# Kernel tuning notes

Measured on AMD Instinct MI355X. Metric: run time of the kernel, lower is better.

The kernel has to match this reference:

```python
import jax, jax.numpy as jnp
import numpy as np

# Model constants (match init_kwargs)
H, P, N, G, NL, K = 32, 64, 128, 1, 15, 4   # heads, head_dim, state, groups, lambda levels, conv width
HID, T, BATCH = 1024, 1024, 1
INTER = H * P                    # 2048
CONV_DIM = INTER + 2 * G * N     # 2304
PROJ = INTER + CONV_DIM + H * (NL + 1)  # 4864
EPS = 1e-5


def _level_matrix(t_len: int) -> np.ndarray:
    """Fenwick-tree level assignment: for query t, prefix [0,t] splits into
    power-of-two segments from binary expansion of t+1; segment of length 2^l -> level l."""
    lm = np.zeros((t_len, t_len), dtype=np.int32)
    for t in range(t_len):
        n = t + 1
        while n > 0:
            lb = n & (-n)
            lm[t, n - lb:n] = lb.bit_length() - 1
            n -= lb
    return lm


def setup_inputs() -> dict:
    key = jax.random.key(0)
    ks = jax.random.split(key, 4)
    return {
        "hidden_states": jax.random.normal(ks[0], (BATCH, T, HID), jnp.float32),
        "in_proj_w": jax.random.normal(ks[1], (PROJ, HID), jnp.float32) / np.sqrt(HID).astype(np.float32),
        "in_proj_b": jnp.zeros((PROJ,), jnp.float32),
        "conv_w": jax.random.normal(ks[2], (CONV_DIM, K), jnp.float32) / np.sqrt(K).astype(np.float32),
        "dt_bias": jnp.ones((H,), jnp.float32),
        "A_log": jnp.log(jnp.arange(1, H + 1, dtype=jnp.float32)),
        "L_param": jnp.ones((H, NL), jnp.float32),
        "D": jnp.ones((H,), jnp.float32),
        "rmsnorm_w": jnp.ones((INTER,), jnp.float32),
        "out_proj_w": jax.random.normal(ks[3], (HID, INTER), jnp.float32) / np.sqrt(INTER).astype(np.float32),
        "out_proj_b": jnp.zeros((HID,), jnp.float32),
        "level_mat": jnp.asarray(_level_matrix(T)),  # (T,T) int32, data-independent
    }


def reference(hidden_states, in_proj_w, in_proj_b, conv_w, dt_bias, A_log,
              L_param, D, rmsnorm_w, out_proj_w, out_proj_b, level_mat):
    b, t, _ = hidden_states.shape
    # in_proj and split: [z | xBC | dt | dl]
    zxbcdtdl = hidden_states @ in_proj_w.T + in_proj_b
    z, xBC, dt, dl = jnp.split(zxbcdtdl, [INTER, INTER + CONV_DIM, INTER + CONV_DIM + H], axis=-1)
    # depthwise causal conv1d (width K) + SiLU
    xp = jnp.pad(xBC, ((0, 0), (K - 1, 0), (0, 0)))
    conv = sum(xp[:, w:w + t, :] * conv_w[:, w] for w in range(K))
    xBC = jax.nn.silu(conv)
    x, Bm, Cm = jnp.split(xBC, [INTER, INTER + G * N], axis=-1)
    x = x.reshape(b, t, H, P)          # v pre-scale
    Bm = Bm.reshape(b, t, G, N)        # keys
    Cm = Cm.reshape(b, t, G, N)        # queries
    dl = dl.reshape(b, t, H, NL)
    # D residual uses unscaled x (matches hmamba_chunk_scan_combined ordering)
    D_res = x * D[None, None, :, None]
    dt = jax.nn.softplus(dt + dt_bias)            # (b,t,H)
    v = x * dt[..., None]                          # (b,t,H,P)
    A = -jnp.exp(A_log)                            # (H,)
    g = A * dt                                     # (b,t,H), per-token log-decay (<=0)
    Ls = jax.nn.softplus(L_param * dl)             # (b,t,H,NL) per-token level scales
    # cumulative log-decay; decay(t,s) = exp(cg_t - cg_s), s<=t
    cg = jnp.cumsum(g, axis=1).transpose(0, 2, 1)  # (b,H,t)
    mask = jnp.tril(jnp.ones((t, t), bool))
    logdecay = jnp.where(mask, cg[:, :, :, None] - cg[:, :, None, :], -jnp.inf)
    decay = jnp.exp(logdecay)                      # (b,H,t,s)
    # hierarchical level scale H[t,s] = Ls[b,t,h, level(t,s)]
    Hmat = jnp.take_along_axis(Ls.transpose(0, 2, 1, 3), level_mat[None, None, :, :], axis=-1)  # (b,H,t,s)
    scores = jnp.einsum('btgn,bsgn->bgts', Cm, Bm)  # (b,G,t,s), G=1 broadcasts over heads
    att = scores * decay * Hmat                     # (b,H,t,s), masked via decay=0
    y = jnp.einsum('bhts,bshp->bthp', att, v) + D_res
    y = y.reshape(b, t, INTER)
    # gated RMSNorm with norm_before_gate=False: normalize(y * silu(z)) * w
    yg = y * jax.nn.silu(z)
    y = yg * jax.lax.rsqrt(jnp.mean(yg * yg, axis=-1, keepdims=True) + EPS) * rmsnorm_w
    return y @ out_proj_w.T + out_proj_b
```

## Files before the change

### kernel.cpp

```cpp
#include <hip/hip_runtime.h>
#include <hip/hip_bf16.h>
#include <math.h>

#define T_LEN 1024
#define HID 1024
#define NHEAD 32
#define HDIM 64
#define NSTATE 128
#define NLVL 15
#define KCONV 4
#define INTER 2048
#define CONV_DIM 2304
#define PROJ 4864
#define NPROJ16 4352
#define NPROJF 512
#define EPS 1e-5f

typedef __attribute__((ext_vector_type(8))) _Float16 half8;
typedef __attribute__((ext_vector_type(4))) float float4v;
typedef unsigned short ushort_t;

__device__ __forceinline__ float softplus_f(float x) {
  return fmaxf(x, 0.f) + log1pf(expf(-fabsf(x)));
}
__device__ __forceinline__ float silu_f(float x) {
  return x / (1.f + expf(-x));
}
__device__ __forceinline__ ushort_t f2h(float f) {
  union { _Float16 h; ushort_t u; } v;
  v.h = (_Float16)f;
  return v.u;
}
__device__ __forceinline__ float h2f(ushort_t u) {
  union { ushort_t u; _Float16 h; } v;
  v.u = u;
  return (float)v.h;
}
__device__ __forceinline__ void gload_lds16(const void* g, void* l) {
  __builtin_amdgcn_global_load_lds(
      (const __attribute__((address_space(1))) void*)g,
      (__attribute__((address_space(3))) void*)l, 16, 0, 0);
}

#define N4_HS  (T_LEN * HID / 4)
#define N4_WI  (PROJ * HID / 4)
#define N4_WO  (HID * INTER / 4)
__global__ __launch_bounds__(256) void prep_f16(
    const float* __restrict__ hs, const float* __restrict__ wi,
    const float* __restrict__ wo, ushort_t* __restrict__ hsb,
    ushort_t* __restrict__ wib, ushort_t* __restrict__ wob) {
  int i = blockIdx.x * 256 + threadIdx.x;
  const float* src; ushort_t* dst; int j;
  if (i < N4_HS)              { src = hs; dst = hsb; j = i; }
  else if (i < N4_HS + N4_WI) { src = wi; dst = wib; j = i - N4_HS; }
  else                        { src = wo; dst = wob; j = i - N4_HS - N4_WI; }
  float4 v = reinterpret_cast<const float4*>(src)[j];
  union { ushort_t u[4]; unsigned long long ll; } o;
  o.u[0] = f2h(v.x); o.u[1] = f2h(v.y); o.u[2] = f2h(v.z); o.u[3] = f2h(v.w);
  reinterpret_cast<unsigned long long*>(dst)[j] = o.ll;
}

__global__ __launch_bounds__(256) void gemm_in(
    const ushort_t* __restrict__ A, const ushort_t* __restrict__ B,
    const float* __restrict__ bias,
    ushort_t* __restrict__ Ch, float* __restrict__ Cf) {
  const int K = HID;
  __shared__ ushort_t As[2][128][32];
  __shared__ ushort_t Bs[2][128][32];
  const int tid = threadIdx.x;
  const int w = tid >> 6, L = tid & 63;
  const int n0 = blockIdx.x * 128, m0 = blockIdx.y * 128;
  const int mq = (w & 1) * 64, nq = (w >> 1) * 64;
  const int srow = (L >> 2);
  const int sch = (L & 3) * 8;

  float4v acc[4][4];
#pragma unroll
  for (int i = 0; i < 4; ++i)
#pragma unroll
    for (int j = 0; j < 4; ++j) acc[i][j] = (float4v){0.f, 0.f, 0.f, 0.f};

  const int niter = K / 32;
  {
#pragma unroll
    for (int j = 0; j < 2; ++j) {
      int r0 = 16 * (w * 2 + j);
      gload_lds16(A + (size_t)(m0 + r0 + srow) * K + sch, &As[0][r0][0]);
      gload_lds16(B + (size_t)(n0 + r0 + srow) * K + sch, &Bs[0][r0][0]);
    }
  }
  for (int it = 0; it < niter; ++it) {
    __syncthreads();
    if (it + 1 < niter) {
      const int kk = (it + 1) * 32;
      const int nb = (it + 1) & 1;
#pragma unroll
      for (int j = 0; j < 2; ++j) {
        int r0 = 16 * (w * 2 + j);
        gload_lds16(A + (size_t)(m0 + r0 + srow) * K + kk + sch, &As[nb][r0][0]);
        gload_lds16(B + (size_t)(n0 + r0 + srow) * K + kk + sch, &Bs[nb][r0][0]);
      }
    }
    const int cb = it & 1;
    half8 af[4], bf[4];
#pragma unroll
    for (int t = 0; t < 4; ++t) {
      af[t] = *reinterpret_cast<const half8*>(&As[cb][mq + t * 16 + (L & 15)][(L >> 4) * 8]);
      bf[t] = *reinterpret_cast<const half8*>(&Bs[cb][nq + t * 16 + (L & 15)][(L >> 4) * 8]);
    }
#pragma unroll
    for (int mt = 0; mt < 4; ++mt)
#pragma unroll
      for (int nt = 0; nt < 4; ++nt)
        acc[mt][nt] = __builtin_amdgcn_mfma_f32_16x16x32_f16(af[mt], bf[nt], acc[mt][nt], 0, 0, 0);
  }
  const int qrow = (L >> 4) * 4;
  const bool tof16 = (n0 < NPROJ16);
#pragma unroll
  for (int mt = 0; mt < 4; ++mt) {
#pragma unroll
    for (int nt = 0; nt < 4; ++nt) {
      int col = n0 + nq + nt * 16 + (L & 15);
      float bv = bias[col];
#pragma unroll
      for (int r = 0; r < 4; ++r) {
        int row = m0 + mq + mt * 16 + qrow + r;
        float v = acc[mt][nt][r] + bv;
        if (tof16) Ch[(size_t)row * NPROJ16 + col] = f2h(v);
        else       Cf[(size_t)row * NPROJF + (col - NPROJ16)] = v;
      }
    }
  }
}

__global__ __launch_bounds__(256) void gemm_f16_sk(
    const ushort_t* __restrict__ A, const ushort_t* __restrict__ B,
    float* __restrict__ Cpart, int M, int N, int K, int Kc) {
  __shared__ ushort_t As[2][128][32];
  __shared__ ushort_t Bs[2][128][32];
  const int tid = threadIdx.x;
  const int w = tid >> 6, L = tid & 63;
  const int n0 = blockIdx.x * 128, m0 = blockIdx.y * 128;
  const int kbeg = blockIdx.z * Kc;
  float* __restrict__ C = Cpart + (size_t)blockIdx.z * M * N;
  const int mq = (w & 1) * 64, nq = (w >> 1) * 64;
  const int srow = (L >> 2);
  const int sch = (L & 3) * 8;

  float4v acc[4][4];
#pragma unroll
  for (int i = 0; i < 4; ++i)
#pragma unroll
    for (int j = 0; j < 4; ++j) acc[i][j] = (float4v){0.f, 0.f, 0.f, 0.f};

  const int niter = Kc / 32;
  {
    const int kk = kbeg;
#pragma unroll
    for (int j = 0; j < 2; ++j) {
      int r0 = 16 * (w * 2 + j);
      gload_lds16(A + (size_t)(m0 + r0 + srow) * K + kk + sch, &As[0][r0][0]);
      gload_lds16(B + (size_t)(n0 + r0 + srow) * K + kk + sch, &Bs[0][r0][0]);
    }
  }
  for (int it = 0; it < niter; ++it) {
    __syncthreads();
    if (it + 1 < niter) {
      const int kk = kbeg + (it + 1) * 32;
      const int nb = (it + 1) & 1;
#pragma unroll
      for (int j = 0; j < 2; ++j) {
        int r0 = 16 * (w * 2 + j);
        gload_lds16(A + (size_t)(m0 + r0 + srow) * K + kk + sch, &As[nb][r0][0]);
        gload_lds16(B + (size_t)(n0 + r0 + srow) * K + kk + sch, &Bs[nb][r0][0]);
      }
    }
    const int cb = it & 1;
    half8 af[4], bf[4];
#pragma unroll
    for (int t = 0; t < 4; ++t) {
      af[t] = *reinterpret_cast<const half8*>(&As[cb][mq + t * 16 + (L & 15)][(L >> 4) * 8]);
      bf[t] = *reinterpret_cast<const half8*>(&Bs[cb][nq + t * 16 + (L & 15)][(L >> 4) * 8]);
    }
#pragma unroll
    for (int mt = 0; mt < 4; ++mt)
#pragma unroll
      for (int nt = 0; nt < 4; ++nt)
        acc[mt][nt] = __builtin_amdgcn_mfma_f32_16x16x32_f16(af[mt], bf[nt], acc[mt][nt], 0, 0, 0);
  }
  const int qrow = (L >> 4) * 4;
#pragma unroll
  for (int mt = 0; mt < 4; ++mt) {
#pragma unroll
    for (int nt = 0; nt < 4; ++nt) {
      int col = n0 + nq + nt * 16 + (L & 15);
#pragma unroll
      for (int r = 0; r < 4; ++r) {
        int row = m0 + mq + mt * 16 + qrow + r;
        C[(size_t)row * N + col] = acc[mt][nt][r];
      }
    }
  }
}

__global__ __launch_bounds__(256) void reduce_out4(const float* __restrict__ p,
                                                   const float* __restrict__ bias,
                                                   float* __restrict__ out, int MN) {
  int i = blockIdx.x * 256 + threadIdx.x;
  if (i * 4 >= MN) return;
  float4 a = reinterpret_cast<const float4*>(p)[i];
  float4 b = reinterpret_cast<const float4*>(p + MN)[i];
  float4 c = reinterpret_cast<const float4*>(p + 2 * (size_t)MN)[i];
  float4 d = reinterpret_cast<const float4*>(p + 3 * (size_t)MN)[i];
  int col = (i * 4) & (HID - 1);
  float4 bv = *reinterpret_cast<const float4*>(bias + col);
  float4 o;
  o.x = a.x + b.x + c.x + d.x + bv.x;
  o.y = a.y + b.y + c.y + d.y + bv.y;
  o.z = a.z + b.z + c.z + d.z + bv.z;
  o.w = a.w + b.w + c.w + d.w + bv.w;
  reinterpret_cast<float4*>(out)[i] = o;
}

__global__ __launch_bounds__(512) void pointwise_dt(
    const float* __restrict__ zxf, const float* __restrict__ dt_bias,
    const float* __restrict__ A_log, const float* __restrict__ L_param,
    float* __restrict__ dtbuf, float* __restrict__ gT,
    float* __restrict__ Lsbuf) {
  const int t = blockIdx.x;
  const int j = threadIdx.x;
  const size_t ro = (size_t)t * NPROJF;
  if (j < NHEAD * NLVL) {
    float x = L_param[j] * zxf[ro + NHEAD + j];
    Lsbuf[(size_t)t * (NHEAD * NLVL) + j] = softplus_f(x);
  } else {
    int h = j - NHEAD * NLVL;
    float x = zxf[ro + h] + dt_bias[h];
    float dt = softplus_f(x);
    dtbuf[t * NHEAD + h] = dt;
    gT[h * T_LEN + t] = -expf(A_log[h]) * dt;
  }
}

__global__ __launch_bounds__(64) void scan_g(const float* __restrict__ gT,
                                             double* __restrict__ cgd) {
  const int h = blockIdx.x, l = threadIdx.x;
  const float* gr = gT + (size_t)h * T_LEN + l * 16;
  double pre[16];
  double acc = 0.0;
#pragma unroll
  for (int i = 0; i < 16; ++i) { acc += (double)gr[i]; pre[i] = acc; }
  double s = acc;
#pragma unroll
  for (int off = 1; off < 64; off <<= 1) {
    double o = __shfl_up(s, off, 64);
    if (l >= off) s += o;
  }
  const double base = s - acc;
  double* cr = cgd + (size_t)h * T_LEN + l * 16;
#pragma unroll
  for (int i = 0; i < 16; ++i) cr[i] = base + pre[i];
}

__global__ __launch_bounds__(256) void conv_fused(
    const ushort_t* __restrict__ zxh, const float* __restrict__ conv_w,
    const float* __restrict__ dtbuf, const float* __restrict__ Dp,
    ushort_t* __restrict__ vt, float* __restrict__ ybuf,
    ushort_t* __restrict__ Bb, ushort_t* __restrict__ Cb) {
  __shared__ ushort_t Vl[64][68];
  __shared__ float dtl[64];
  const int tq = blockIdx.x, cy = blockIdx.y;
  const int t0 = tq * 64;
  const int tid = threadIdx.x;
  const int lane = tid & 63, g = tid >> 6;
  const bool vpath = (cy < 32);
  const int ccol = vpath ? cy * 64 + lane : INTER + (cy - 32) * 64 + lane;
  const int zcol = INTER + ccol;
  float cw[KCONV];
#pragma unroll
  for (int w = 0; w < KCONV; ++w) cw[w] = conv_w[ccol * KCONV + w];
  if (vpath && tid < 64) dtl[tid] = dtbuf[(t0 + tid) * NHEAD + cy];
  const float Dh = vpath ? Dp[cy] : 0.f;

  float xv[19];
#pragma unroll
  for (int i = 0; i < 19; ++i) {
    int tt = t0 + g * 16 - 3 + i;
    if (tt >= 0) {
      xv[i] = h2f(zxh[(size_t)tt * NPROJ16 + zcol]);
    } else xv[i] = 0.f;
  }
  __syncthreads();
#pragma unroll
  for (int i = 0; i < 16; ++i) {
    float acc = xv[i] * cw[0] + xv[i + 1] * cw[1] + xv[i + 2] * cw[2] + xv[i + 3] * cw[3];
    float sil = silu_f(acc);
    int tl = g * 16 + i;
    int t = t0 + tl;
    if (vpath) {
      ushort_t vh = f2h(sil * dtl[tl]);
      Vl[tl][lane] = vh;
      ybuf[(size_t)t * INTER + cy * 64 + lane] = sil * Dh;
    } else if (ccol < INTER + NSTATE) {
      Bb[t * NSTATE + (ccol - INTER)] = f2h(sil);
    } else {
      Cb[t * NSTATE + (ccol - INTER - NSTATE)] = f2h(sil);
    }
  }
  if (vpath) {
    __syncthreads();
#pragma unroll
    for (int rep = 0; rep < 2; ++rep) {
      int u = tid + 256 * rep;
      int p = u >> 3, t8 = (u & 7) * 8;
      union { ushort_t u16[8]; half8 h; } o;
#pragma unroll
      for (int j = 0; j < 8; ++j) o.u16[j] = Vl[t8 + j][p];
      *reinterpret_cast<half8*>(vt + (size_t)(cy * 64 + p) * T_LEN + t0 + t8) = o.h;
    }
  }
}

__global__ __launch_bounds__(256) void attn_mfma(
    const ushort_t* __restrict__ Bb, const ushort_t* __restrict__ Cb,
    const ushort_t* __restrict__ vt, const double* __restrict__ cgd,
    const float* __restrict__ Lsb, float* __restrict__ ybuf) {
  __shared__ ushort_t Bl[64][136];
  __shared__ ushort_t Vtl[64][72];
  __shared__ ushort_t Sl[64][72];
  __shared__ float Lsl[64][16];
  __shared__ float cgq[64];
  __shared__ float cgs[64];

  const int item = blockIdx.x;
  const int h = item / 40;
  const int rem = item - h * 40;
  int qt, j;
  if (rem < 4)        { qt = rem;                 j = 0; }
  else if (rem < 12)  { qt = 4 + (rem - 4) / 2;   j = (rem - 4) % 2; }
  else if (rem < 24)  { qt = 8 + (rem - 12) / 3;  j = (rem - 12) % 3; }
  else                { qt = 12 + (rem - 24) / 4; j = (rem - 24) % 4; }

  const int tid = threadIdx.x;
  const int w = tid >> 6, L = tid & 63;
  const int tq0 = qt * 64;
  const double* cgh = cgd + (size_t)h * T_LEN;
  const double base = cgh[tq0];

  for (int i = tid; i < 64 * NLVL; i += 256) {
    int r = i / NLVL, l = i - r * NLVL;
    Lsl[r][l] = Lsb[(size_t)(tq0 + r) * (NHEAD * NLVL) + h * NLVL + l];
  }
  if (tid < 64) cgq[tid] = (float)(cgh[tq0 + tid] - base);

  half8 cfrag[4];
  {
    const ushort_t* cr = Cb + (size_t)(tq0 + w * 16 + (L & 15)) * NSTATE + (L >> 4) * 8;
#pragma unroll
    for (int ks = 0; ks < 4; ++ks)
      cfrag[ks] = *reinterpret_cast<const half8*>(cr + ks * 32);
  }
  float4v yac[4];
#pragma unroll
  for (int i = 0; i < 4; ++i) yac[i] = (float4v){0.f, 0.f, 0.f, 0.f};

  const int qrow = w * 16 + ((L >> 4) << 2);

  const int st0 = 4 * j;
  const int st1 = min(4 * j + 4, qt + 1);
  for (int st = st0; st < st1; ++st) {
    const int ts0 = st * 64;
    __syncthreads();
#pragma unroll
    for (int i = 0; i < 4; ++i) {
      int u = tid + 256 * i;
      int row = u >> 4, kb = (u & 15) * 8;
      *reinterpret_cast<half8*>(&Bl[row][kb]) =
          *reinterpret_cast<const half8*>(Bb + (size_t)(ts0 + row) * NSTATE + kb);
    }
#pragma unroll
    for (int i = 0; i < 2; ++i) {
      int u = tid + 256 * i;
      int p = u >> 3, sc = (u & 7) * 8;
      *reinterpret_cast<half8*>(&Vtl[p][sc]) =
          *reinterpret_cast<const half8*>(vt + (size_t)(h * HDIM + p) * T_LEN + ts0 + sc);
    }
    if (tid < 64) cgs[tid] = (float)(cgh[ts0 + tid] - base);
    __syncthreads();

    float4v sac[4];
#pragma unroll
    for (int nt = 0; nt < 4; ++nt) sac[nt] = (float4v){0.f, 0.f, 0.f, 0.f};
#pragma unroll
    for (int ks = 0; ks < 4; ++ks) {
#pragma unroll
      for (int nt = 0; nt < 4; ++nt) {
        half8 bfrag = *reinterpret_cast<const half8*>(&Bl[nt * 16 + (L & 15)][ks * 32 + (L >> 4) * 8]);
        sac[nt] = __builtin_amdgcn_mfma_f32_16x16x32_f16(cfrag[ks], bfrag, sac[nt], 0, 0, 0);
      }
    }
#pragma unroll
    for (int nt = 0; nt < 4; ++nt) {
      int s = nt * 16 + (L & 15);
      int sg = ts0 + s;
      float cs = cgs[s];
#pragma unroll
      for (int r = 0; r < 4; ++r) {
        int q = qrow + r;
        int tg = tq0 + q;
        float val = 0.f;
        if (sg <= tg) {
          int lvl = 31 - __clz((unsigned)(sg ^ (tg + 1)));
          val = sac[nt][r] * __expf(cgq[q] - cs) * Lsl[q][lvl];
        }
        Sl[q][s] = f2h(val);
      }
    }
    __builtin_amdgcn_s_waitcnt(0);
#pragma unroll
    for (int ks = 0; ks < 2; ++ks) {
      half8 af = *reinterpret_cast<const half8*>(&Sl[w * 16 + (L & 15)][ks * 32 + (L >> 4) * 8]);
#pragma unroll
      for (int pt = 0; pt < 4; ++pt) {
        half8 bfv = *reinterpret_cast<const half8*>(&Vtl[pt * 16 + (L & 15)][ks * 32 + (L >> 4) * 8]);
        yac[pt] = __builtin_amdgcn_mfma_f32_16x16x32_f16(af, bfv, yac[pt], 0, 0, 0);
      }
    }
  }
#pragma unroll
  for (int pt = 0; pt < 4; ++pt) {
    int p = pt * 16 + (L & 15);
#pragma unroll
    for (int r = 0; r < 4; ++r) {
      int q = qrow + r;
      atomicAdd(ybuf + (size_t)(tq0 + q) * INTER + h * HDIM + p, yac[pt][r]);
    }
  }
}

__global__ __launch_bounds__(256) void rmsnorm_gate(
    const float* __restrict__ ybuf, const ushort_t* __restrict__ zxh,
    const float* __restrict__ w, ushort_t* __restrict__ yhf) {
  __shared__ float red[4];
  const int t = blockIdx.x, tid = threadIdx.x;
  const size_t ro = (size_t)t * NPROJ16;
  const float* yrow = ybuf + (size_t)t * INTER;
  float yg[8];
  float ss = 0.f;
#pragma unroll
  for (int i = 0; i < 8; ++i) {
    int c = tid + 256 * i;
    float z = h2f(zxh[ro + c]);
    float g = yrow[c] * silu_f(z);
    yg[i] = g;
    ss += g * g;
  }
#pragma unroll
  for (int off = 32; off; off >>= 1) ss += __shfl_down(ss, off, 64);
  if ((tid & 63) == 0) red[tid >> 6] = ss;
  __syncthreads();
  if (tid == 0) red[0] = red[0] + red[1] + red[2] + red[3];
  __syncthreads();
  const float scale = rsqrtf(red[0] / (float)INTER + EPS);
#pragma unroll
  for (int i = 0; i < 8; ++i) {
    int c = tid + 256 * i;
    yhf[(size_t)t * INTER + c] = f2h(yg[i] * scale * w[c]);
  }
}

extern "C" void kernel_launch(void* const* d_in, const int* in_sizes, int n_in,
                              void* d_out, int out_size, void* d_ws, size_t ws_size,
                              hipStream_t stream) {
  const float* hs        = (const float*)d_in[0];
  const float* in_proj_w = (const float*)d_in[1];
  const float* in_proj_b = (const float*)d_in[2];
  const float* conv_w    = (const float*)d_in[3];
  const float* dt_bias   = (const float*)d_in[4];
  const float* A_log     = (const float*)d_in[5];
  const float* L_param   = (const float*)d_in[6];
  const float* Dp        = (const float*)d_in[7];
  const float* rms_w     = (const float*)d_in[8];
  const float* out_proj_w= (const float*)d_in[9];
  const float* out_proj_b= (const float*)d_in[10];
  float* out = (float*)d_out;

  char* W = (char*)d_ws;
  size_t off = 0;
  auto alloc = [&](size_t bytes) { void* p = W + off; off = (off + bytes + 255) & ~(size_t)255; return p; };
  double*   cgd = (double*)  alloc((size_t)NHEAD * T_LEN * 8);
  float*    zxf = (float*)   alloc((size_t)T_LEN * NPROJF * 4);
  float*    opp = (float*)   alloc((size_t)4 * T_LEN * HID * 4);
  float*    ybuf= (float*)   alloc((size_t)T_LEN * INTER * 4);
  float*    gT  = (float*)   alloc((size_t)NHEAD * T_LEN * 4);
  float*    dtb = (float*)   alloc((size_t)T_LEN * NHEAD * 4);
  float*    Lsb = (float*)   alloc((size_t)T_LEN * NHEAD * NLVL * 4);
  ushort_t* zxh = (ushort_t*)alloc((size_t)T_LEN * NPROJ16 * 2);
  ushort_t* hsb = (ushort_t*)alloc((size_t)T_LEN * HID * 2);
  ushort_t* Wib = (ushort_t*)alloc((size_t)PROJ * HID * 2);
  ushort_t* Wob = (ushort_t*)alloc((size_t)HID * INTER * 2);
  ushort_t* yhf = (ushort_t*)alloc((size_t)T_LEN * INTER * 2);
  ushort_t* vt  = (ushort_t*)alloc((size_t)T_LEN * INTER * 2);
  ushort_t* Bb  = (ushort_t*)alloc((size_t)T_LEN * NSTATE * 2);
  ushort_t* Cb  = (ushort_t*)alloc((size_t)T_LEN * NSTATE * 2);

  prep_f16<<<(N4_HS + N4_WI + N4_WO) / 256, 256, 0, stream>>>(
      hs, in_proj_w, out_proj_w, hsb, Wib, Wob);

  gemm_in<<<dim3(PROJ / 128, T_LEN / 128), 256, 0, stream>>>(
      hsb, Wib, in_proj_b, zxh, zxf);

  pointwise_dt<<<T_LEN, 512, 0, stream>>>(zxf, dt_bias, A_log, L_param, dtb, gT, Lsb);

  scan_g<<<NHEAD, 64, 0, stream>>>(gT, cgd);

  conv_fused<<<dim3(T_LEN / 64, 36), 256, 0, stream>>>(
      zxh, conv_w, dtb, Dp, vt, ybuf, Bb, Cb);

  attn_mfma<<<NHEAD * 40, 256, 0, stream>>>(Bb, Cb, vt, cgd, Lsb, ybuf);

  rmsnorm_gate<<<T_LEN, 256, 0, stream>>>(ybuf, zxh, rms_w, yhf);

  gemm_f16_sk<<<dim3(HID / 128, T_LEN / 128, 4), 256, 0, stream>>>(
      yhf, Wob, opp, T_LEN, HID, INTER, INTER / 4);
  reduce_out4<<<(T_LEN * HID / 4 + 255) / 256, 256, 0, stream>>>(
      opp, out_proj_b, out, T_LEN * HID);
}
```

Before: 206.0 us.

## Hoist shared C·B score GEMM out of per-head attention and widen GEMM K-tiles

Because G=1, the C·B^T score matrix is identical across all 32 heads. It is now computed once by a new qk_gemm kernel into a T×T fp16 buffer, and attn_mfma reads it directly into registers instead of recomputing it per head. The masked decay/level scaling is done in registers, which removes the LDS round trip through Sl. Separately, both dense GEMMs move to 64-wide K tiles with an XOR-swizzled LDS layout to halve the number of barriers and avoid bank conflicts. The trade-offs are an extra launch, a 2MB intermediate buffer re-read by every head, and higher LDS use per GEMM block.

```diff
diff --git a/kernel.cpp b/kernel.cpp
--- a/kernel.cpp
+++ b/kernel.cpp
@@ -65,14 +65,14 @@
     const float* __restrict__ bias,
     ushort_t* __restrict__ Ch, float* __restrict__ Cf) {
   const int K = HID;
-  __shared__ ushort_t As[2][128][32];
-  __shared__ ushort_t Bs[2][128][32];
+  __shared__ ushort_t As[2][128][64];
+  __shared__ ushort_t Bs[2][128][64];
   const int tid = threadIdx.x;
   const int w = tid >> 6, L = tid & 63;
   const int n0 = blockIdx.x * 128, m0 = blockIdx.y * 128;
   const int mq = (w & 1) * 64, nq = (w >> 1) * 64;
-  const int srow = (L >> 2);
-  const int sch = (L & 3) * 8;
+  const int srow = L >> 3;
+  const int swst = ((L & 7) ^ srow) * 8;
 
   float4v acc[4][4];
 #pragma unroll
@@ -80,39 +80,46 @@
 #pragma unroll
     for (int j = 0; j < 4; ++j) acc[i][j] = (float4v){0.f, 0.f, 0.f, 0.f};
 
-  const int niter = K / 32;
+  const int niter = K / 64;
   {
 #pragma unroll
-    for (int j = 0; j < 2; ++j) {
-      int r0 = 16 * (w * 2 + j);
-      gload_lds16(A + (size_t)(m0 + r0 + srow) * K + sch, &As[0][r0][0]);
-      gload_lds16(B + (size_t)(n0 + r0 + srow) * K + sch, &Bs[0][r0][0]);
+    for (int j = 0; j < 4; ++j) {
+      int r0 = 8 * (w * 4 + j);
+      gload_lds16(A + (size_t)(m0 + r0 + srow) * K + swst, &As[0][r0][0]);
+      gload_lds16(B + (size_t)(n0 + r0 + srow) * K + swst, &Bs[0][r0][0]);
     }
   }
   for (int it = 0; it < niter; ++it) {
     __syncthreads();
     if (it + 1 < niter) {
-      const int kk = (it + 1) * 32;
+      const int kk = (it + 1) * 64;
       const int nb = (it + 1) & 1;
 #pragma unroll
-      for (int j = 0; j < 2; ++j) {
-        int r0 = 16 * (w * 2 + j);
-        gload_lds16(A + (size_t)(m0 + r0 + srow) * K + kk + sch, &As[nb][r0][0]);
-        gload_lds16(B + (size_t)(n0 + r0 + srow) * K + kk + sch, &Bs[nb][r0][0]);
+      for (int j = 0; j < 4; ++j) {
+        int r0 = 8 * (w * 4 + j);
+        gload_lds16(A + (size_t)(m0 + r0 + srow) * K + kk + swst, &As[nb][r0][0]);
+        gload_lds16(B + (size_t)(n0 + r0 + srow) * K + kk + swst, &Bs[nb][r0][0]);
       }
     }
     const int cb = it & 1;
-    half8 af[4], bf[4];
-#pragma unroll
-    for (int t = 0; t < 4; ++t) {
-      af[t] = *reinterpret_cast<const half8*>(&As[cb][mq + t * 16 + (L & 15)][(L >> 4) * 8]);
-      bf[t] = *reinterpret_cast<const half8*>(&Bs[cb][nq + t * 16 + (L & 15)][(L >> 4) * 8]);
-    }
-#pragma unroll
-    for (int mt = 0; mt < 4; ++mt)
-#pragma unroll
-      for (int nt = 0; nt < 4; ++nt)
-        acc[mt][nt] = __builtin_amdgcn_mfma_f32_16x16x32_f16(af[mt], bf[nt], acc[mt][nt], 0, 0, 0);
+    half8 af[4][2], bf[4][2];
+#pragma unroll
+    for (int kk2 = 0; kk2 < 2; ++kk2) {
+      const int sw = ((kk2 * 4 + (L >> 4)) ^ (L & 7)) * 8;
+#pragma unroll
+      for (int t = 0; t < 4; ++t) {
+        af[t][kk2] = *reinterpret_cast<const half8*>(&As[cb][mq + t * 16 + (L & 15)][sw]);
+        bf[t][kk2] = *reinterpret_cast<const half8*>(&Bs[cb][nq + t * 16 + (L & 15)][sw]);
+      }
+    }
+#pragma unroll
+    for (int kk2 = 0; kk2 < 2; ++kk2)
+#pragma unroll
+      for (int mt = 0; mt < 4; ++mt)
+#pragma unroll
+        for (int nt = 0; nt < 4; ++nt)
+          acc[mt][nt] = __builtin_amdgcn_mfma_f32_16x16x32_f16(af[mt][kk2], bf[nt][kk2],
+                                                               acc[mt][nt], 0, 0, 0);
   }
   const int qrow = (L >> 4) * 4;
   const bool tof16 = (n0 < NPROJ16);
@@ -136,16 +143,16 @@
 __global__ __launch_bounds__(256) void gemm_f16_sk(
     const ushort_t* __restrict__ A, const ushort_t* __restrict__ B,
     float* __restrict__ Cpart, int M, int N, int K, int Kc) {
-  __shared__ ushort_t As[2][128][32];
-  __shared__ ushort_t Bs[2][128][32];
+  __shared__ ushort_t As[2][128][64];
+  __shared__ ushort_t Bs[2][128][64];
   const int tid = threadIdx.x;
   const int w = tid >> 6, L = tid & 63;
   const int n0 = blockIdx.x * 128, m0 = blockIdx.y * 128;
   const int kbeg = blockIdx.z * Kc;
   float* __restrict__ C = Cpart + (size_t)blockIdx.z * M * N;
   const int mq = (w & 1) * 64, nq = (w >> 1) * 64;
-  const int srow = (L >> 2);
-  const int sch = (L & 3) * 8;
+  const int srow = L >> 3;
+  const int swst = ((L & 7) ^ srow) * 8;
 
   float4v acc[4][4];
 #pragma unroll
@@ -153,40 +160,46 @@
 #pragma unroll
     for (int j = 0; j < 4; ++j) acc[i][j] = (float4v){0.f, 0.f, 0.f, 0.f};
 
-  const int niter = Kc / 32;
+  const int niter = Kc / 64;
   {
-    const int kk = kbeg;
-#pragma unroll
-    for (int j = 0; j < 2; ++j) {
-      int r0 = 16 * (w * 2 + j);
-      gload_lds16(A + (size_t)(m0 + r0 + srow) * K + kk + sch, &As[0][r0][0]);
-      gload_lds16(B + (size_t)(n0 + r0 + srow) * K + kk + sch, &Bs[0][r0][0]);
+#pragma unroll
+    for (int j = 0; j < 4; ++j) {
+      int r0 = 8 * (w * 4 + j);
+      gload_lds16(A + (size_t)(m0 + r0 + srow) * K + kbeg + swst, &As[0][r0][0]);
+      gload_lds16(B + (size_t)(n0 + r0 + srow) * K + kbeg + swst, &Bs[0][r0][0]);
     }
   }
   for (int it = 0; it < niter; ++it) {
     __syncthreads();
     if (it + 1 < niter) {
-      const int kk = kbeg + (it + 1) * 32;
+      const int kk = kbeg + (it + 1) * 64;
       const int nb = (it + 1) & 1;
 #pragma unroll
-      for (int j = 0; j < 2; ++j) {
-        int r0 = 16 * (w * 2 + j);
-        gload_lds16(A + (size_t)(m0 + r0 + srow) * K + kk + sch, &As[nb][r0][0]);
-        gload_lds16(B + (size_t)(n0 + r0 + srow) * K + kk + sch, &Bs[nb][r0][0]);
+      for (int j = 0; j < 4; ++j) {
+        int r0 = 8 * (w * 4 + j);
+        gload_lds16(A + (size_t)(m0 + r0 + srow) * K + kk + swst, &As[nb][r0][0]);
+        gload_lds16(B + (size_t)(n0 + r0 + srow) * K + kk + swst, &Bs[nb][r0][0]);
       }
     }
     const int cb = it & 1;
-    half8 af[4], bf[4];
-#pragma unroll
-    for (int t = 0; t < 4; ++t) {
-      af[t] = *reinterpret_cast<const half8*>(&As[cb][mq + t * 16 + (L & 15)][(L >> 4) * 8]);
-      bf[t] = *reinterpret_cast<const half8*>(&Bs[cb][nq + t * 16 + (L & 15)][(L >> 4) * 8]);
-    }
-#pragma unroll
-    for (int mt = 0; mt < 4; ++mt)
-#pragma unroll
-      for (int nt = 0; nt < 4; ++nt)
-        acc[mt][nt] = __builtin_amdgcn_mfma_f32_16x16x32_f16(af[mt], bf[nt], acc[mt][nt], 0, 0, 0);
+    half8 af[4][2], bf[4][2];
+#pragma unroll
+    for (int kk2 = 0; kk2 < 2; ++kk2) {
+      const int sw = ((kk2 * 4 + (L >> 4)) ^ (L & 7)) * 8;
+#pragma unroll
+      for (int t = 0; t < 4; ++t) {
+        af[t][kk2] = *reinterpret_cast<const half8*>(&As[cb][mq + t * 16 + (L & 15)][sw]);
+        bf[t][kk2] = *reinterpret_cast<const half8*>(&Bs[cb][nq + t * 16 + (L & 15)][sw]);
+      }
+    }
+#pragma unroll
+    for (int kk2 = 0; kk2 < 2; ++kk2)
+#pragma unroll
+      for (int mt = 0; mt < 4; ++mt)
+#pragma unroll
+        for (int nt = 0; nt < 4; ++nt)
+          acc[mt][nt] = __builtin_amdgcn_mfma_f32_16x16x32_f16(af[mt][kk2], bf[nt][kk2],
+                                                               acc[mt][nt], 0, 0, 0);
   }
   const int qrow = (L >> 4) * 4;
 #pragma unroll
@@ -321,16 +334,61 @@
   }
 }
 
+__global__ __launch_bounds__(256) void qk_gemm(
+    const ushort_t* __restrict__ Cq, const ushort_t* __restrict__ Bk,
+    ushort_t* __restrict__ S) {
+  const int idx = blockIdx.x;
+  int qt = (int)(0.5f * (sqrtf(8.f * (float)idx + 1.f) - 1.f));
+  if ((qt + 1) * (qt + 2) / 2 <= idx) ++qt;
+  if (qt * (qt + 1) / 2 > idx) --qt;
+  const int st = idx - qt * (qt + 1) / 2;
+  const int tid = threadIdx.x, w = tid >> 6, L = tid & 63;
+  const int q0 = qt * 64 + (w & 1) * 32;
+  const int s0 = st * 64 + (w >> 1) * 32;
+
+  half8 af[2][4], bf[2][4];
+#pragma unroll
+  for (int mt = 0; mt < 2; ++mt)
+#pragma unroll
+    for (int ks = 0; ks < 4; ++ks) {
+      af[mt][ks] = *reinterpret_cast<const half8*>(
+          Cq + (size_t)(q0 + mt * 16 + (L & 15)) * NSTATE + ks * 32 + (L >> 4) * 8);
+      bf[mt][ks] = *reinterpret_cast<const half8*>(
+          Bk + (size_t)(s0 + mt * 16 + (L & 15)) * NSTATE + ks * 32 + (L >> 4) * 8);
+    }
+  float4v acc[2][2];
+#pragma unroll
+  for (int i = 0; i < 2; ++i)
+#pragma unroll
+    for (int j = 0; j < 2; ++j) acc[i][j] = (float4v){0.f, 0.f, 0.f, 0.f};
+#pragma unroll
+  for (int ks = 0; ks < 4; ++ks)
+#pragma unroll
+    for (int mt = 0; mt < 2; ++mt)
+#pragma unroll
+      for (int nt = 0; nt < 2; ++nt)
+        acc[mt][nt] = __builtin_amdgcn_mfma_f32_16x16x32_f16(af[mt][ks], bf[nt][ks],
+                                                             acc[mt][nt], 0, 0, 0);
+  const int qrow = (L >> 4) * 4;
+#pragma unroll
+  for (int mt = 0; mt < 2; ++mt)
+#pragma unroll
+    for (int nt = 0; nt < 2; ++nt) {
+      int col = s0 + nt * 16 + (L & 15);
+#pragma unroll
+      for (int r = 0; r < 4; ++r)
+        S[(size_t)(q0 + mt * 16 + qrow + r) * T_LEN + col] = f2h(acc[mt][nt][r]);
+    }
+}
+
 __global__ __launch_bounds__(256) void attn_mfma(
-    const ushort_t* __restrict__ Bb, const ushort_t* __restrict__ Cb,
-    const ushort_t* __restrict__ vt, const double* __restrict__ cgd,
-    const float* __restrict__ Lsb, float* __restrict__ ybuf) {
-  __shared__ ushort_t Bl[64][136];
+    const ushort_t* __restrict__ S, const ushort_t* __restrict__ vt,
+    const double* __restrict__ cgd, const float* __restrict__ Lsb,
+    float* __restrict__ ybuf) {
   __shared__ ushort_t Vtl[64][72];
-  __shared__ ushort_t Sl[64][72];
-  __shared__ float Lsl[64][16];
-  __shared__ float cgq[64];
-  __shared__ float cgs[64];
+  __shared__ float Lsl[64][17];
+  __shared__ __align__(16) float cgq[64];
+  __shared__ __align__(16) float cgs[64];
 
   const int item = blockIdx.x;
   const int h = item / 40;
@@ -353,17 +411,12 @@
   }
   if (tid < 64) cgq[tid] = (float)(cgh[tq0 + tid] - base);
 
-  half8 cfrag[4];
-  {
-    const ushort_t* cr = Cb + (size_t)(tq0 + w * 16 + (L & 15)) * NSTATE + (L >> 4) * 8;
-#pragma unroll
-    for (int ks = 0; ks < 4; ++ks)
-      cfrag[ks] = *reinterpret_cast<const half8*>(cr + ks * 32);
-  }
   float4v yac[4];
 #pragma unroll
   for (int i = 0; i < 4; ++i) yac[i] = (float4v){0.f, 0.f, 0.f, 0.f};
 
+  const int qloc = w * 16 + (L & 15);
+  const int tg = tq0 + qloc;
   const int qrow = w * 16 + ((L >> 4) << 2);
 
   const int st0 = 4 * j;
@@ -371,13 +424,10 @@
   for (int st = st0; st < st1; ++st) {
     const int ts0 = st * 64;
     __syncthreads();
-#pragma unroll
-    for (int i = 0; i < 4; ++i) {
-      int u = tid + 256 * i;
-      int row = u >> 4, kb = (u & 15) * 8;
-      *reinterpret_cast<half8*>(&Bl[row][kb]) =
-          *reinterpret_cast<const half8*>(Bb + (size_t)(ts0 + row) * NSTATE + kb);
-    }
+    half8 sv0 = *reinterpret_cast<const half8*>(
+        S + (size_t)tg * T_LEN + ts0 + (L >> 4) * 8);
+    half8 sv1 = *reinterpret_cast<const half8*>(
+        S + (size_t)tg * T_LEN + ts0 + 32 + (L >> 4) * 8);
 #pragma unroll
     for (int i = 0; i < 2; ++i) {
       int u = tid + 256 * i;
@@ -388,42 +438,34 @@
     if (tid < 64) cgs[tid] = (float)(cgh[ts0 + tid] - base);
     __syncthreads();
 
-    float4v sac[4];
-#pragma unroll
-    for (int nt = 0; nt < 4; ++nt) sac[nt] = (float4v){0.f, 0.f, 0.f, 0.f};
-#pragma unroll
-    for (int ks = 0; ks < 4; ++ks) {
-#pragma unroll
-      for (int nt = 0; nt < 4; ++nt) {
-        half8 bfrag = *reinterpret_cast<const half8*>(&Bl[nt * 16 + (L & 15)][ks * 32 + (L >> 4) * 8]);
-        sac[nt] = __builtin_amdgcn_mfma_f32_16x16x32_f16(cfrag[ks], bfrag, sac[nt], 0, 0, 0);
-      }
-    }
-#pragma unroll
-    for (int nt = 0; nt < 4; ++nt) {
-      int s = nt * 16 + (L & 15);
-      int sg = ts0 + s;
-      float cs = cgs[s];
-#pragma unroll
-      for (int r = 0; r < 4; ++r) {
-        int q = qrow + r;
-        int tg = tq0 + q;
+    const float cq = cgq[qloc];
+    half8 af[2];
+#pragma unroll
+    for (int ks = 0; ks < 2; ++ks) {
+      const half8 sv = ks ? sv1 : sv0;
+      const int sb = ks * 32 + (L >> 4) * 8;
+      float4 c0 = *reinterpret_cast<const float4*>(&cgs[sb]);
+      float4 c1 = *reinterpret_cast<const float4*>(&cgs[sb + 4]);
+      float csv[8] = {c0.x, c0.y, c0.z, c0.w, c1.x, c1.y, c1.z, c1.w};
+      union { ushort_t u[8]; half8 h; } o;
+#pragma unroll
+      for (int jj = 0; jj < 8; ++jj) {
+        int sg = ts0 + sb + jj;
         float val = 0.f;
         if (sg <= tg) {
           int lvl = 31 - __clz((unsigned)(sg ^ (tg + 1)));
-          val = sac[nt][r] * __expf(cgq[q] - cs) * Lsl[q][lvl];
+          val = (float)sv[jj] * __expf(cq - csv[jj]) * Lsl[qloc][lvl];
         }
-        Sl[q][s] = f2h(val);
-      }
-    }
-    __builtin_amdgcn_s_waitcnt(0);
+        o.u[jj] = f2h(val);
+      }
+      af[ks] = o.h;
+    }
 #pragma unroll
     for (int ks = 0; ks < 2; ++ks) {
-      half8 af = *reinterpret_cast<const half8*>(&Sl[w * 16 + (L & 15)][ks * 32 + (L >> 4) * 8]);
 #pragma unroll
       for (int pt = 0; pt < 4; ++pt) {
         half8 bfv = *reinterpret_cast<const half8*>(&Vtl[pt * 16 + (L & 15)][ks * 32 + (L >> 4) * 8]);
-        yac[pt] = __builtin_amdgcn_mfma_f32_16x16x32_f16(af, bfv, yac[pt], 0, 0, 0);
+        yac[pt] = __builtin_amdgcn_mfma_f32_16x16x32_f16(af[ks], bfv, yac[pt], 0, 0, 0);
       }
     }
   }
@@ -503,6 +545,7 @@
   ushort_t* vt  = (ushort_t*)alloc((size_t)T_LEN * INTER * 2);
   ushort_t* Bb  = (ushort_t*)alloc((size_t)T_LEN * NSTATE * 2);
   ushort_t* Cb  = (ushort_t*)alloc((size_t)T_LEN * NSTATE * 2);
+  ushort_t* Sbuf= (ushort_t*)alloc((size_t)T_LEN * T_LEN * 2);
 
   prep_f16<<<(N4_HS + N4_WI + N4_WO) / 256, 256, 0, stream>>>(
       hs, in_proj_w, out_proj_w, hsb, Wib, Wob);
@@ -517,7 +560,9 @@
   conv_fused<<<dim3(T_LEN / 64, 36), 256, 0, stream>>>(
       zxh, conv_w, dtb, Dp, vt, ybuf, Bb, Cb);
 
-  attn_mfma<<<NHEAD * 40, 256, 0, stream>>>(Bb, Cb, vt, cgd, Lsb, ybuf);
+  qk_gemm<<<136, 256, 0, stream>>>(Cb, Bb, Sbuf);
+
+  attn_mfma<<<NHEAD * 40, 256, 0, stream>>>(Sbuf, vt, cgd, Lsb, ybuf);
 
   rmsnorm_gate<<<T_LEN, 256, 0, stream>>>(ybuf, zxh, rms_w, yhf);
 
```

Result: faster. 192.0 us (median of 2 runs) (-6.8%).
